# Kernel optimization log

Measured on AMD Instinct MI355X. Metric: run time of the kernel, lower is better.

## Reference

```python
import jax, jax.numpy as jnp
import numpy as np

N = 100000
E = 1600000
NEG_SLOPE = 0.2


def gat_layer(x, W, al, ar, b, src, dst):
    """DGL GATConv (no dropout, no residual, bias=True, activation=None).
    x: [N, in]; W: [in, H*D]; al, ar, b: [H, D]. Returns [N, H, D]."""
    H, D = al.shape
    feat = (x @ W).reshape(N, H, D)               # [N,H,D]
    el = jnp.sum(feat * al, axis=-1)              # [N,H]
    er = jnp.sum(feat * ar, axis=-1)              # [N,H]
    e = jax.nn.leaky_relu(el[src] + er[dst], NEG_SLOPE)  # [E,H]
    # segment softmax over incoming edges of each dst node
    emax = jax.lax.stop_gradient(jax.ops.segment_max(e, dst, num_segments=N))
    ex = jnp.exp(e - emax[dst])                   # [E,H]
    denom = jax.ops.segment_sum(ex, dst, num_segments=N)  # [N,H]
    alpha = ex / jnp.where(denom[dst] == 0, 1.0, denom[dst])  # [E,H]
    msg = feat[src] * alpha[..., None]            # [E,H,D] gather + weight
    out = jax.ops.segment_sum(msg, dst, num_segments=N)    # [N,H,D] scatter-add
    return out + b[None, :, :]


def setup_inputs() -> dict:
    key = jax.random.key(0)
    ks = jax.random.split(key, 12)
    in_size, hid, out_size, heads = 128, 32, 16, 4
    x = jax.random.normal(ks[0], (N, in_size), dtype=jnp.float32)
    src = jax.random.randint(ks[1], (E,), 0, N, dtype=jnp.int32)
    dst = jax.random.randint(ks[2], (E,), 0, N, dtype=jnp.int32)
    W1 = jax.random.normal(ks[3], (in_size, heads * hid), dtype=jnp.float32) * (1.0 / np.sqrt(in_size))
    al1 = jax.random.normal(ks[4], (heads, hid), dtype=jnp.float32) * 0.1
    ar1 = jax.random.normal(ks[5], (heads, hid), dtype=jnp.float32) * 0.1
    b1 = jnp.zeros((heads, hid), dtype=jnp.float32)
    W2 = jax.random.normal(ks[6], (hid, out_size), dtype=jnp.float32) * (1.0 / np.sqrt(hid))
    al2 = jax.random.normal(ks[7], (1, out_size), dtype=jnp.float32) * 0.1
    ar2 = jax.random.normal(ks[8], (1, out_size), dtype=jnp.float32) * 0.1
    b2 = jnp.zeros((1, out_size), dtype=jnp.float32)
    return {"x": x, "src": src, "dst": dst, "W1": W1, "al1": al1, "ar1": ar1,
            "b1": b1, "W2": W2, "al2": al2, "ar2": ar2, "b2": b2}


def reference(x, src, dst, W1, al1, ar1, b1, W2, al2, ar2, b2):
    h = gat_layer(x, W1, al1, ar1, b1, src, dst)   # [N, heads, hid]
    h = jax.nn.relu(jnp.mean(h, axis=1))           # mean over heads + relu
    h = gat_layer(h, W2, al2, ar2, b2, src, dst)   # [N, 1, out]
    return h.reshape(N, -1)                        # flatten
```

## Files before the change

kernel.cpp:

```cpp
#include <hip/hip_runtime.h>
#include <hip/hip_bf16.h>

#define NEG_SLOPE 0.2f
#define G_SHIFT 7
#define GSZ 128
#define CHUNK 4096

__global__ __launch_bounds__(256) void coarse_scatter(
    const int* __restrict__ src, const int* __restrict__ dst,
    int* __restrict__ gcursor, unsigned* __restrict__ inter, int NB, int E) {
    __shared__ int hist[800];
    __shared__ int lbase[800];
    __shared__ int gbase[800];
    __shared__ unsigned stage[CHUNK];
    __shared__ unsigned short bstage[CHUNK];

    const int tid = threadIdx.x;
    const int e0 = blockIdx.x * CHUNK;
    const int cnt = min(CHUNK, E - e0);

    for (int i = tid; i < NB; i += 256) hist[i] = 0;
    __syncthreads();

    unsigned pk[16];
    int bb[16];
#pragma unroll
    for (int r = 0; r < 16; ++r) {
        int idx = tid + r * 256;
        if (idx < cnt) {
            int s = src[e0 + idx];
            int d = dst[e0 + idx];
            pk[r] = ((unsigned)s << G_SHIFT) | (unsigned)(d & (GSZ - 1));
            bb[r] = d >> G_SHIFT;
            atomicAdd(&hist[bb[r]], 1);
        }
    }
    __syncthreads();
    if (tid < 64) {
        int carry = 0;
        for (int i = 0; i < NB; i += 64) {
            int v = (i + tid < NB) ? hist[i + tid] : 0;
            int xv = v;
            for (int o = 1; o < 64; o <<= 1) {
                int tt = __shfl_up(xv, o, 64);
                if (tid >= o) xv += tt;
            }
            if (i + tid < NB) lbase[i + tid] = carry + xv - v;
            carry += __shfl(xv, 63, 64);
        }
    }
    __syncthreads();
    for (int i = tid; i < NB; i += 256) {
        int hh = hist[i];
        gbase[i] = (hh > 0) ? (i * CHUNK + atomicAdd(&gcursor[i], hh)) : 0;
    }
    __syncthreads();
    for (int i = tid; i < NB; i += 256) hist[i] = 0;
    __syncthreads();
#pragma unroll
    for (int r = 0; r < 16; ++r) {
        int idx = tid + r * 256;
        if (idx < cnt) {
            int b = bb[r];
            int rk = atomicAdd(&hist[b], 1);
            int pos = lbase[b] + rk;
            stage[pos] = pk[r];
            bstage[pos] = (unsigned short)b;
        }
    }
    __syncthreads();
#pragma unroll
    for (int r = 0; r < 16; ++r) {
        int idx = tid + r * 256;
        if (idx < cnt) {
            int b = (int)bstage[idx];
            inter[gbase[b] + (idx - lbase[b])] = stage[idx];
        }
    }
}

__global__ __launch_bounds__(256) void fine_scatter(
    const unsigned* __restrict__ inter, const int* __restrict__ gcursor,
    int* __restrict__ deg, int* __restrict__ rowptr, int* __restrict__ esrc,
    int N, int NB) {
    __shared__ int h[GSZ];
    __shared__ int lb[GSZ];
    __shared__ int stage[CHUNK];
    __shared__ int redsum[256];
    const int b = blockIdx.x;
    const int tid = threadIdx.x;
    const int cnt = gcursor[b];
    const unsigned* ep = inter + (size_t)b * CHUNK;

    {
        int s = 0;
        for (int i = tid; i < b; i += 256) s += gcursor[i];
        redsum[tid] = s;
        __syncthreads();
        for (int o = 128; o > 0; o >>= 1) {
            if (tid < o) redsum[tid] += redsum[tid + o];
            __syncthreads();
        }
    }
    const int base = redsum[0];

    if (tid < GSZ) h[tid] = 0;
    __syncthreads();

    int ss[16];
    unsigned char ln[16];
    int nr = 0;
    for (int idx = tid; idx < cnt; idx += 256) {
        unsigned ed = ep[idx];
        ss[nr] = (int)(ed >> G_SHIFT);
        int l = (int)(ed & (GSZ - 1));
        ln[nr++] = (unsigned char)l;
        atomicAdd(&h[l], 1);
    }
    __syncthreads();
    if (tid < 64) {
        int carry = 0;
        for (int i = 0; i < GSZ; i += 64) {
            int v = h[i + tid];
            int xv = v;
            for (int o = 1; o < 64; o <<= 1) {
                int tt = __shfl_up(xv, o, 64);
                if (tid >= o) xv += tt;
            }
            lb[i + tid] = carry + xv - v;
            carry += __shfl(xv, 63, 64);
        }
    }
    __syncthreads();
    if (tid < GSZ) {
        int node = b * GSZ + tid;
        if (node < N) {
            deg[node] = h[tid];
            rowptr[node] = base + lb[tid];
        }
        h[tid] = 0;
    }
    __syncthreads();
    for (int r = 0; r < nr; ++r) {
        int l = ln[r];
        int rk = atomicAdd(&h[l], 1);
        stage[lb[l] + rk] = ss[r];
    }
    __syncthreads();
    for (int idx = tid; idx < cnt; idx += 256) esrc[base + idx] = stage[idx];
}

__global__ __launch_bounds__(256) void gemm1_fused(
    const float* __restrict__ x, const float* __restrict__ W,
    const float* __restrict__ al, const float* __restrict__ ar,
    __hip_bfloat16* __restrict__ outb, float* __restrict__ el,
    float* __restrict__ er, int N) {
    const int K = 128, C = 128, BK = 32;
    __shared__ float xs[BK][68];
    __shared__ float ws[BK][C];

    const int t = threadIdx.x;
    const int trow = t >> 4;
    const int tcol = t & 15;
    const int m0 = blockIdx.x * 64;

    float acc[4][8];
#pragma unroll
    for (int i = 0; i < 4; ++i)
#pragma unroll
        for (int j = 0; j < 8; ++j) acc[i][j] = 0.f;

    for (int k0 = 0; k0 < K; k0 += BK) {
        {
            const float4* W4 = (const float4*)(W + k0 * C);
#pragma unroll
            for (int r = 0; r < 4; ++r) {
                int q = t + 256 * r;
                int k = q >> 5;
                int c4 = q & 31;
                float4 v = W4[k * 32 + c4];
                *((float4*)&ws[k][c4 * 4]) = v;
            }
        }
        {
#pragma unroll
            for (int r = 0; r < 2; ++r) {
                int q = t + 256 * r;
                int m = q >> 3;
                int k4 = q & 7;
                int gm = m0 + m;
                if (gm >= N) gm = N - 1;
                float4 v = *((const float4*)(x + (size_t)gm * K + k0 + k4 * 4));
                xs[k4 * 4 + 0][m] = v.x;
                xs[k4 * 4 + 1][m] = v.y;
                xs[k4 * 4 + 2][m] = v.z;
                xs[k4 * 4 + 3][m] = v.w;
            }
        }
        __syncthreads();

#pragma unroll
        for (int k = 0; k < BK; ++k) {
            float4 a = *((const float4*)&xs[k][trow * 4]);
            float4 b0 = *((const float4*)&ws[k][tcol * 8]);
            float4 b1 = *((const float4*)&ws[k][tcol * 8 + 4]);
            float av[4] = {a.x, a.y, a.z, a.w};
            float bv[8] = {b0.x, b0.y, b0.z, b0.w, b1.x, b1.y, b1.z, b1.w};
#pragma unroll
            for (int i = 0; i < 4; ++i)
#pragma unroll
                for (int j = 0; j < 8; ++j) acc[i][j] += av[i] * bv[j];
        }
        __syncthreads();
    }

    const int h = tcol >> 2;
    const int d0 = (tcol & 3) * 8;
    float alv[8], arv[8];
#pragma unroll
    for (int j = 0; j < 8; ++j) {
        alv[j] = al[h * 32 + d0 + j];
        arv[j] = ar[h * 32 + d0 + j];
    }
#pragma unroll
    for (int i = 0; i < 4; ++i) {
        int gm = m0 + trow * 4 + i;
        if (gm < N) {
            union { __hip_bfloat16 hh[8]; uint4 u; } pk;
#pragma unroll
            for (int j = 0; j < 8; ++j) pk.hh[j] = __float2bfloat16(acc[i][j]);
            *((uint4*)(outb + (size_t)gm * C + tcol * 8)) = pk.u;
        }
        float pl = 0.f, pr = 0.f;
#pragma unroll
        for (int j = 0; j < 8; ++j) {
            pl += acc[i][j] * alv[j];
            pr += acc[i][j] * arv[j];
        }
        pl += __shfl_xor(pl, 1); pl += __shfl_xor(pl, 2);
        pr += __shfl_xor(pr, 1); pr += __shfl_xor(pr, 2);
        if ((tcol & 3) == 0 && gm < N) {
            el[gm * 4 + h] = pl;
            er[gm * 4 + h] = pr;
        }
    }
}

__device__ __forceinline__ float bf2f(unsigned short v) {
    return __uint_as_float((unsigned)v << 16);
}

__global__ __launch_bounds__(256) void pull1_kernel(
    const int* __restrict__ rowptr, const int* __restrict__ deg,
    const int* __restrict__ esrc, const float* __restrict__ el,
    const float* __restrict__ er, const __hip_bfloat16* __restrict__ featb,
    const float* __restrict__ b,
    const float* __restrict__ W2, const float* __restrict__ al2,
    const float* __restrict__ ar2, float* __restrict__ feat2,
    float* __restrict__ el2, float* __restrict__ er2, int N) {
    int tid = blockIdx.x * 256 + threadIdx.x;
    int node = tid >> 5;
    int lane = threadIdx.x & 31;
    int h = lane >> 3;
    int d4 = lane & 7;
    if (node >= N) return;

    int start = rowptr[node];
    int cnt = deg[node];
    float er_nh = er[node * 4 + h];
    const int* ep = esrc + start;
    const unsigned short* fb = (const unsigned short*)featb + h * 32 + d4 * 4;

    float4 acc = make_float4(0.f, 0.f, 0.f, 0.f);
    float sumex = 0.f;

    int i = 0;
    for (; i + 4 <= cnt; i += 4) {
        int s0 = ep[i], s1 = ep[i + 1], s2 = ep[i + 2], s3 = ep[i + 3];
        float e0 = el[s0 * 4 + h], e1 = el[s1 * 4 + h];
        float e2 = el[s2 * 4 + h], e3 = el[s3 * 4 + h];
        ushort4 u0 = *((const ushort4*)(fb + (size_t)s0 * 128));
        ushort4 u1 = *((const ushort4*)(fb + (size_t)s1 * 128));
        ushort4 u2 = *((const ushort4*)(fb + (size_t)s2 * 128));
        ushort4 u3 = *((const ushort4*)(fb + (size_t)s3 * 128));
        float v0 = e0 + er_nh; v0 = v0 > 0.f ? v0 : NEG_SLOPE * v0;
        float v1 = e1 + er_nh; v1 = v1 > 0.f ? v1 : NEG_SLOPE * v1;
        float v2 = e2 + er_nh; v2 = v2 > 0.f ? v2 : NEG_SLOPE * v2;
        float v3 = e3 + er_nh; v3 = v3 > 0.f ? v3 : NEG_SLOPE * v3;
        float x0 = __expf(v0), x1 = __expf(v1), x2 = __expf(v2), x3 = __expf(v3);
        acc.x += x0 * bf2f(u0.x); acc.y += x0 * bf2f(u0.y);
        acc.z += x0 * bf2f(u0.z); acc.w += x0 * bf2f(u0.w);
        acc.x += x1 * bf2f(u1.x); acc.y += x1 * bf2f(u1.y);
        acc.z += x1 * bf2f(u1.z); acc.w += x1 * bf2f(u1.w);
        acc.x += x2 * bf2f(u2.x); acc.y += x2 * bf2f(u2.y);
        acc.z += x2 * bf2f(u2.z); acc.w += x2 * bf2f(u2.w);
        acc.x += x3 * bf2f(u3.x); acc.y += x3 * bf2f(u3.y);
        acc.z += x3 * bf2f(u3.z); acc.w += x3 * bf2f(u3.w);
        sumex += x0 + x1 + x2 + x3;
    }
    for (; i < cnt; ++i) {
        int s = ep[i];
        float v = el[s * 4 + h] + er_nh;
        v = v > 0.f ? v : NEG_SLOPE * v;
        float ex = __expf(v);
        ushort4 u = *((const ushort4*)(fb + (size_t)s * 128));
        acc.x += ex * bf2f(u.x); acc.y += ex * bf2f(u.y);
        acc.z += ex * bf2f(u.z); acc.w += ex * bf2f(u.w);
        sumex += ex;
    }
    float inv = 1.f / ((sumex == 0.f) ? 1.f : sumex);
    float4 bb = *((const float4*)(b + h * 32 + d4 * 4));
    float4 o;
    o.x = acc.x * inv + bb.x;
    o.y = acc.y * inv + bb.y;
    o.z = acc.z * inv + bb.z;
    o.w = acc.w * inv + bb.w;
    o.x += __shfl_xor(o.x, 8); o.x += __shfl_xor(o.x, 16);
    o.y += __shfl_xor(o.y, 8); o.y += __shfl_xor(o.y, 16);
    o.z += __shfl_xor(o.z, 8); o.z += __shfl_xor(o.z, 16);
    o.w += __shfl_xor(o.w, 8); o.w += __shfl_xor(o.w, 16);
    float4 hb;
    hb.x = fmaxf(o.x * 0.25f, 0.f);
    hb.y = fmaxf(o.y * 0.25f, 0.f);
    hb.z = fmaxf(o.z * 0.25f, 0.f);
    hb.w = fmaxf(o.w * 0.25f, 0.f);

    int c = lane & 15;
    const float* w2c = W2 + c;
    float fc = 0.f;
#pragma unroll
    for (int j = 0; j < 8; ++j) {
        float4 hbj;
        hbj.x = __shfl(hb.x, j, 32);
        hbj.y = __shfl(hb.y, j, 32);
        hbj.z = __shfl(hb.z, j, 32);
        hbj.w = __shfl(hb.w, j, 32);
        fc += hbj.x * w2c[(j * 4 + 0) * 16];
        fc += hbj.y * w2c[(j * 4 + 1) * 16];
        fc += hbj.z * w2c[(j * 4 + 2) * 16];
        fc += hbj.w * w2c[(j * 4 + 3) * 16];
    }
    float pl = fc * al2[c];
    float pr = fc * ar2[c];
    pl += __shfl_xor(pl, 1, 32); pl += __shfl_xor(pl, 2, 32);
    pl += __shfl_xor(pl, 4, 32); pl += __shfl_xor(pl, 8, 32);
    pr += __shfl_xor(pr, 1, 32); pr += __shfl_xor(pr, 2, 32);
    pr += __shfl_xor(pr, 4, 32); pr += __shfl_xor(pr, 8, 32);
    if (lane < 16) feat2[(size_t)node * 16 + c] = fc;
    if (lane == 0) {
        el2[node] = pl;
        er2[node] = pr;
    }
}

__global__ __launch_bounds__(256) void pull2_kernel(
    const int* __restrict__ rowptr, const int* __restrict__ deg,
    const int* __restrict__ esrc, const float* __restrict__ el,
    const float* __restrict__ er, const float* __restrict__ feat,
    const float* __restrict__ b, float* __restrict__ outp, int N) {
    int tid = blockIdx.x * 256 + threadIdx.x;
    int node = tid >> 2;
    int d4 = threadIdx.x & 3;
    if (node >= N) return;

    int start = rowptr[node];
    int cnt = deg[node];
    float er_n = er[node];
    const int* ep = esrc + start;
    const float* fb = feat + d4 * 4;

    float4 acc = make_float4(0.f, 0.f, 0.f, 0.f);
    float sumex = 0.f;
    int i = 0;
    for (; i + 8 <= cnt; i += 8) {
        int s[8];
#pragma unroll
        for (int j = 0; j < 8; ++j) s[j] = ep[i + j];
        float ee[8];
        float4 ff[8];
#pragma unroll
        for (int j = 0; j < 8; ++j) {
            ee[j] = el[s[j]];
            ff[j] = *((const float4*)(fb + (size_t)s[j] * 16));
        }
#pragma unroll
        for (int j = 0; j < 8; ++j) {
            float v = ee[j] + er_n;
            v = v > 0.f ? v : NEG_SLOPE * v;
            float ex = __expf(v);
            acc.x += ex * ff[j].x; acc.y += ex * ff[j].y;
            acc.z += ex * ff[j].z; acc.w += ex * ff[j].w;
            sumex += ex;
        }
    }
    for (; i + 4 <= cnt; i += 4) {
        int s[4];
#pragma unroll
        for (int j = 0; j < 4; ++j) s[j] = ep[i + j];
        float ee[4];
        float4 ff[4];
#pragma unroll
        for (int j = 0; j < 4; ++j) {
            ee[j] = el[s[j]];
            ff[j] = *((const float4*)(fb + (size_t)s[j] * 16));
        }
#pragma unroll
        for (int j = 0; j < 4; ++j) {
            float v = ee[j] + er_n;
            v = v > 0.f ? v : NEG_SLOPE * v;
            float ex = __expf(v);
            acc.x += ex * ff[j].x; acc.y += ex * ff[j].y;
            acc.z += ex * ff[j].z; acc.w += ex * ff[j].w;
            sumex += ex;
        }
    }
    for (; i < cnt; ++i) {
        int s = ep[i];
        float v = el[s] + er_n;
        v = v > 0.f ? v : NEG_SLOPE * v;
        float ex = __expf(v);
        float4 f = *((const float4*)(fb + (size_t)s * 16));
        acc.x += ex * f.x; acc.y += ex * f.y;
        acc.z += ex * f.z; acc.w += ex * f.w;
        sumex += ex;
    }
    float inv = 1.f / ((sumex == 0.f) ? 1.f : sumex);
    float4 bb = *((const float4*)(b + d4 * 4));
    float4 o;
    o.x = acc.x * inv + bb.x;
    o.y = acc.y * inv + bb.y;
    o.z = acc.z * inv + bb.z;
    o.w = acc.w * inv + bb.w;
    *((float4*)(outp + (size_t)node * 16 + d4 * 4)) = o;
}

extern "C" void kernel_launch(void* const* d_in, const int* in_sizes, int n_in,
                              void* d_out, int out_size, void* d_ws, size_t ws_size,
                              hipStream_t stream) {
    const float* x   = (const float*)d_in[0];
    const int*   src = (const int*)d_in[1];
    const int*   dst = (const int*)d_in[2];
    const float* W1  = (const float*)d_in[3];
    const float* al1 = (const float*)d_in[4];
    const float* ar1 = (const float*)d_in[5];
    const float* b1  = (const float*)d_in[6];
    const float* W2  = (const float*)d_in[7];
    const float* al2 = (const float*)d_in[8];
    const float* ar2 = (const float*)d_in[9];
    const float* b2  = (const float*)d_in[10];

    const int E = in_sizes[1];
    const int N = in_sizes[0] / 128;
    const int H1 = 4, C1 = 128;
    const int D2 = 16;
    const int NB = (N + GSZ - 1) / GSZ;
    const int NCH = (E + CHUNK - 1) / CHUNK;

    char* p = (char*)d_ws;
    auto alloc_f = [&](size_t n) { float* q = (float*)p; p += n * sizeof(float); return q; };
    auto alloc_i = [&](size_t n) { int* q = (int*)p; p += n * sizeof(int); return q; };

    __hip_bfloat16* feat1b = (__hip_bfloat16*)p; p += (size_t)N * C1 * sizeof(__hip_bfloat16);
    float* el1   = alloc_f((size_t)N * H1);
    float* er1   = alloc_f((size_t)N * H1);
    float* feat2 = alloc_f((size_t)N * D2);
    float* el2   = alloc_f(N);
    float* er2   = alloc_f(N);
    int* deg     = alloc_i(N);
    int* rowptr  = alloc_i(N);
    int* esrc    = alloc_i(E);
    int* gcursor = alloc_i(NB);
    unsigned* inter = (unsigned*)alloc_i((size_t)NB * CHUNK);

    const int TB = 256;
    auto blocks = [&](long long n) { return (int)((n + TB - 1) / TB); };

    hipMemsetAsync(gcursor, 0, (size_t)NB * sizeof(int), stream);
    coarse_scatter<<<NCH, TB, 0, stream>>>(src, dst, gcursor, inter, NB, E);
    fine_scatter<<<NB, TB, 0, stream>>>(inter, gcursor, deg, rowptr, esrc, N, NB);

    gemm1_fused<<<(N + 63) / 64, TB, 0, stream>>>(x, W1, al1, ar1, feat1b, el1, er1, N);
    pull1_kernel<<<blocks((long long)N * 32), TB, 0, stream>>>(
        rowptr, deg, esrc, el1, er1, feat1b, b1,
        W2, al2, ar2, feat2, el2, er2, N);

    pull2_kernel<<<blocks((long long)N * 4), TB, 0, stream>>>(
        rowptr, deg, esrc, el2, er2, feat2, b2, (float*)d_out, N);
}
```

Baseline: 284.6 us.

## Dedupe per-edge exp across lanes via shuffles and remap GEMM column layout

In both aggregation kernels, each lane now computes the leaky-relu and exp for only one (edge, head) pair and broadcasts it with shuffles. Before, every lane recomputed all of them redundantly, repeating the el gathers and exp work. The GEMM epilogue changes each thread's columns from 8 contiguous values to two 4-wide groups 64 apart, which changes the LDS read pattern and the bf16 stores and needs an extra shuffle reduction step. Layer 2 also drops its 4-wide unrolled tail loop, so more edges go through the scalar remainder loop.

```diff
diff --git a/kernel.cpp b/kernel.cpp
--- a/kernel.cpp
+++ b/kernel.cpp
@@ -202,8 +202,8 @@
 #pragma unroll
         for (int k = 0; k < BK; ++k) {
             float4 a = *((const float4*)&xs[k][trow * 4]);
-            float4 b0 = *((const float4*)&ws[k][tcol * 8]);
-            float4 b1 = *((const float4*)&ws[k][tcol * 8 + 4]);
+            float4 b0 = *((const float4*)&ws[k][tcol * 4]);
+            float4 b1 = *((const float4*)&ws[k][tcol * 4 + 64]);
             float av[4] = {a.x, a.y, a.z, a.w};
             float bv[8] = {b0.x, b0.y, b0.z, b0.w, b1.x, b1.y, b1.z, b1.w};
 #pragma unroll
@@ -214,34 +214,47 @@
         __syncthreads();
     }
 
-    const int h = tcol >> 2;
-    const int d0 = (tcol & 3) * 8;
-    float alv[8], arv[8];
-#pragma unroll
-    for (int j = 0; j < 8; ++j) {
-        alv[j] = al[h * 32 + d0 + j];
-        arv[j] = ar[h * 32 + d0 + j];
+    const int hA = tcol >> 3;
+    const int hB = hA + 2;
+    const int dOff = (tcol & 7) * 4;
+    float alA[4], arA[4], alB[4], arB[4];
+#pragma unroll
+    for (int j = 0; j < 4; ++j) {
+        alA[j] = al[hA * 32 + dOff + j];
+        arA[j] = ar[hA * 32 + dOff + j];
+        alB[j] = al[hB * 32 + dOff + j];
+        arB[j] = ar[hB * 32 + dOff + j];
     }
 #pragma unroll
     for (int i = 0; i < 4; ++i) {
         int gm = m0 + trow * 4 + i;
         if (gm < N) {
-            union { __hip_bfloat16 hh[8]; uint4 u; } pk;
-#pragma unroll
-            for (int j = 0; j < 8; ++j) pk.hh[j] = __float2bfloat16(acc[i][j]);
-            *((uint4*)(outb + (size_t)gm * C + tcol * 8)) = pk.u;
-        }
-        float pl = 0.f, pr = 0.f;
-#pragma unroll
-        for (int j = 0; j < 8; ++j) {
-            pl += acc[i][j] * alv[j];
-            pr += acc[i][j] * arv[j];
-        }
-        pl += __shfl_xor(pl, 1); pl += __shfl_xor(pl, 2);
-        pr += __shfl_xor(pr, 1); pr += __shfl_xor(pr, 2);
-        if ((tcol & 3) == 0 && gm < N) {
-            el[gm * 4 + h] = pl;
-            er[gm * 4 + h] = pr;
+            union { __hip_bfloat16 hh[4]; uint2 u; } pA, pB;
+#pragma unroll
+            for (int j = 0; j < 4; ++j) {
+                pA.hh[j] = __float2bfloat16(acc[i][j]);
+                pB.hh[j] = __float2bfloat16(acc[i][j + 4]);
+            }
+            *((uint2*)(outb + (size_t)gm * C + tcol * 4)) = pA.u;
+            *((uint2*)(outb + (size_t)gm * C + tcol * 4 + 64)) = pB.u;
+        }
+        float plA = 0.f, prA = 0.f, plB = 0.f, prB = 0.f;
+#pragma unroll
+        for (int j = 0; j < 4; ++j) {
+            plA += acc[i][j] * alA[j];
+            prA += acc[i][j] * arA[j];
+            plB += acc[i][j + 4] * alB[j];
+            prB += acc[i][j + 4] * arB[j];
+        }
+        plA += __shfl_xor(plA, 1); plA += __shfl_xor(plA, 2); plA += __shfl_xor(plA, 4);
+        prA += __shfl_xor(prA, 1); prA += __shfl_xor(prA, 2); prA += __shfl_xor(prA, 4);
+        plB += __shfl_xor(plB, 1); plB += __shfl_xor(plB, 2); plB += __shfl_xor(plB, 4);
+        prB += __shfl_xor(prB, 1); prB += __shfl_xor(prB, 2); prB += __shfl_xor(prB, 4);
+        if ((tcol & 7) == 0 && gm < N) {
+            el[gm * 4 + hA] = plA;
+            er[gm * 4 + hA] = prA;
+            el[gm * 4 + hB] = plB;
+            er[gm * 4 + hB] = prB;
         }
     }
 }
@@ -263,13 +276,17 @@
     int lane = threadIdx.x & 31;
     int h = lane >> 3;
     int d4 = lane & 7;
+    int jrole = lane & 3;
+    int hrole = (lane >> 2) & 3;
     if (node >= N) return;
 
     int start = rowptr[node];
     int cnt = deg[node];
+    float er_c = er[node * 4 + hrole];
     float er_nh = er[node * 4 + h];
     const int* ep = esrc + start;
     const unsigned short* fb = (const unsigned short*)featb + h * 32 + d4 * 4;
+    const int sbase = h << 2;
 
     float4 acc = make_float4(0.f, 0.f, 0.f, 0.f);
     float sumex = 0.f;
@@ -277,17 +294,21 @@
     int i = 0;
     for (; i + 4 <= cnt; i += 4) {
         int s0 = ep[i], s1 = ep[i + 1], s2 = ep[i + 2], s3 = ep[i + 3];
-        float e0 = el[s0 * 4 + h], e1 = el[s1 * 4 + h];
-        float e2 = el[s2 * 4 + h], e3 = el[s3 * 4 + h];
+        int sa = (jrole & 1) ? s1 : s0;
+        int sb = (jrole & 1) ? s3 : s2;
+        int sj = (jrole & 2) ? sb : sa;
+        float ee = el[sj * 4 + hrole];
         ushort4 u0 = *((const ushort4*)(fb + (size_t)s0 * 128));
         ushort4 u1 = *((const ushort4*)(fb + (size_t)s1 * 128));
         ushort4 u2 = *((const ushort4*)(fb + (size_t)s2 * 128));
         ushort4 u3 = *((const ushort4*)(fb + (size_t)s3 * 128));
-        float v0 = e0 + er_nh; v0 = v0 > 0.f ? v0 : NEG_SLOPE * v0;
-        float v1 = e1 + er_nh; v1 = v1 > 0.f ? v1 : NEG_SLOPE * v1;
-        float v2 = e2 + er_nh; v2 = v2 > 0.f ? v2 : NEG_SLOPE * v2;
-        float v3 = e3 + er_nh; v3 = v3 > 0.f ? v3 : NEG_SLOPE * v3;
-        float x0 = __expf(v0), x1 = __expf(v1), x2 = __expf(v2), x3 = __expf(v3);
+        float vv = ee + er_c;
+        vv = vv > 0.f ? vv : NEG_SLOPE * vv;
+        float myex = __expf(vv);
+        float x0 = __shfl(myex, sbase + 0, 32);
+        float x1 = __shfl(myex, sbase + 1, 32);
+        float x2 = __shfl(myex, sbase + 2, 32);
+        float x3 = __shfl(myex, sbase + 3, 32);
         acc.x += x0 * bf2f(u0.x); acc.y += x0 * bf2f(u0.y);
         acc.z += x0 * bf2f(u0.z); acc.w += x0 * bf2f(u0.w);
         acc.x += x1 * bf2f(u1.x); acc.y += x1 * bf2f(u1.y);
@@ -373,46 +394,37 @@
     float sumex = 0.f;
     int i = 0;
     for (; i + 8 <= cnt; i += 8) {
-        int s[8];
-#pragma unroll
-        for (int j = 0; j < 8; ++j) s[j] = ep[i + j];
-        float ee[8];
-        float4 ff[8];
-#pragma unroll
-        for (int j = 0; j < 8; ++j) {
-            ee[j] = el[s[j]];
-            ff[j] = *((const float4*)(fb + (size_t)s[j] * 16));
-        }
-#pragma unroll
-        for (int j = 0; j < 8; ++j) {
-            float v = ee[j] + er_n;
-            v = v > 0.f ? v : NEG_SLOPE * v;
-            float ex = __expf(v);
-            acc.x += ex * ff[j].x; acc.y += ex * ff[j].y;
-            acc.z += ex * ff[j].z; acc.w += ex * ff[j].w;
-            sumex += ex;
-        }
-    }
-    for (; i + 4 <= cnt; i += 4) {
-        int s[4];
-#pragma unroll
-        for (int j = 0; j < 4; ++j) s[j] = ep[i + j];
-        float ee[4];
-        float4 ff[4];
-#pragma unroll
-        for (int j = 0; j < 4; ++j) {
-            ee[j] = el[s[j]];
-            ff[j] = *((const float4*)(fb + (size_t)s[j] * 16));
-        }
-#pragma unroll
-        for (int j = 0; j < 4; ++j) {
-            float v = ee[j] + er_n;
-            v = v > 0.f ? v : NEG_SLOPE * v;
-            float ex = __expf(v);
-            acc.x += ex * ff[j].x; acc.y += ex * ff[j].y;
-            acc.z += ex * ff[j].z; acc.w += ex * ff[j].w;
-            sumex += ex;
-        }
+        int s0 = ep[i], s1 = ep[i + 1], s2 = ep[i + 2], s3 = ep[i + 3];
+        int s4 = ep[i + 4], s5 = ep[i + 5], s6 = ep[i + 6], s7 = ep[i + 7];
+        int sa = (d4 & 1) ? s1 : s0, sb = (d4 & 1) ? s3 : s2;
+        int sA = (d4 & 2) ? sb : sa;
+        int sc = (d4 & 1) ? s5 : s4, sd = (d4 & 1) ? s7 : s6;
+        int sB = (d4 & 2) ? sd : sc;
+        float eA = el[sA], eB = el[sB];
+        float4 f0 = *((const float4*)(fb + (size_t)s0 * 16));
+        float4 f1 = *((const float4*)(fb + (size_t)s1 * 16));
+        float4 f2 = *((const float4*)(fb + (size_t)s2 * 16));
+        float4 f3 = *((const float4*)(fb + (size_t)s3 * 16));
+        float4 f4 = *((const float4*)(fb + (size_t)s4 * 16));
+        float4 f5 = *((const float4*)(fb + (size_t)s5 * 16));
+        float4 f6 = *((const float4*)(fb + (size_t)s6 * 16));
+        float4 f7 = *((const float4*)(fb + (size_t)s7 * 16));
+        float vA = eA + er_n; vA = vA > 0.f ? vA : NEG_SLOPE * vA;
+        float vB = eB + er_n; vB = vB > 0.f ? vB : NEG_SLOPE * vB;
+        float exA = __expf(vA), exB = __expf(vB);
+        float x0 = __shfl(exA, 0, 4), x1 = __shfl(exA, 1, 4);
+        float x2 = __shfl(exA, 2, 4), x3 = __shfl(exA, 3, 4);
+        float x4 = __shfl(exB, 0, 4), x5 = __shfl(exB, 1, 4);
+        float x6 = __shfl(exB, 2, 4), x7 = __shfl(exB, 3, 4);
+        acc.x += x0 * f0.x; acc.y += x0 * f0.y; acc.z += x0 * f0.z; acc.w += x0 * f0.w;
+        acc.x += x1 * f1.x; acc.y += x1 * f1.y; acc.z += x1 * f1.z; acc.w += x1 * f1.w;
+        acc.x += x2 * f2.x; acc.y += x2 * f2.y; acc.z += x2 * f2.z; acc.w += x2 * f2.w;
+        acc.x += x3 * f3.x; acc.y += x3 * f3.y; acc.z += x3 * f3.z; acc.w += x3 * f3.w;
+        acc.x += x4 * f4.x; acc.y += x4 * f4.y; acc.z += x4 * f4.z; acc.w += x4 * f4.w;
+        acc.x += x5 * f5.x; acc.y += x5 * f5.y; acc.z += x5 * f5.z; acc.w += x5 * f5.w;
+        acc.x += x6 * f6.x; acc.y += x6 * f6.y; acc.z += x6 * f6.z; acc.w += x6 * f6.w;
+        acc.x += x7 * f7.x; acc.y += x7 * f7.y; acc.z += x7 * f7.z; acc.w += x7 * f7.w;
+        sumex += x0 + x1 + x2 + x3 + x4 + x5 + x6 + x7;
     }
     for (; i < cnt; ++i) {
         int s = ep[i];
```

Result: slower. 294.1 us (+3.3%).
